# Kernel tuning notes

Measured on AMD Instinct MI355X. Metric: run time of the kernel, lower is better.

Reference implementation:

```python
import jax, jax.numpy as jnp
import numpy as np

B, T, C, H = 4, 4096, 1024, 128

def setup_inputs() -> dict:
    key = jax.random.key(0)
    kx, kq, kk, kv = jax.random.split(key, 4)
    s = 1.0 / np.sqrt(C)  # linear-layer-like init scale
    return {
        "x": jax.random.normal(kx, (B, T, C), dtype=jnp.float32),
        "Wq": jax.random.normal(kq, (C, H), dtype=jnp.float32) * s,
        "Wk": jax.random.normal(kk, (C, H), dtype=jnp.float32) * s,
        "Wv": jax.random.normal(kv, (C, H), dtype=jnp.float32) * s,
    }

def reference(x, Wq, Wk, Wv):
    # q,k,v: [B,T,H]
    q = jnp.einsum('btc,ch->bth', x, Wq)
    k = jnp.einsum('btc,ch->bth', x, Wk)
    v = jnp.einsum('btc,ch->bth', x, Wv)
    # scores: [B,T,T]  (NOTE: source applies no 1/sqrt(H) scaling)
    wei = jnp.einsum('bth,bih->bti', q, k)
    t = x.shape[1]
    causal = jnp.tril(jnp.ones((t, t), dtype=bool))
    wei = jnp.where(causal, wei, -jnp.inf)
    probs = jax.nn.softmax(wei, axis=-1)
    out = jnp.einsum('btj,bjh->bth', probs, v)
    return out
```

## Files before the change

kernel.cpp:

```cpp
#include <hip/hip_runtime.h>

#define B_ 4
#define T_ 4096
#define C_ 1024
#define H_ 128

typedef __attribute__((ext_vector_type(8))) __bf16 bf16x8;
typedef __attribute__((ext_vector_type(8))) unsigned short u16x8;
typedef __attribute__((ext_vector_type(4))) float f32x4;

__device__ __forceinline__ unsigned short f2bf(float f) {
  unsigned int u = __float_as_uint(f);
  return (unsigned short)((u + 0x7FFFu + ((u >> 16) & 1u)) >> 16);
}
__device__ __forceinline__ float bf2f(unsigned short h) {
  return __uint_as_float((unsigned)h << 16);
}
__device__ __forceinline__ bf16x8 ldb8(const unsigned short* p) {
  return *(const bf16x8*)(const void*)p;
}
__device__ __forceinline__ void async16(void* lds, const void* g) {
  __builtin_amdgcn_global_load_lds(
      (const __attribute__((address_space(1))) unsigned int*)g,
      (__attribute__((address_space(3))) unsigned int*)lds, 16, 0, 0);
}
__device__ __forceinline__ void split8a(const float* f, bf16x8& hi, bf16x8& lo) {
  u16x8 h, l;
#pragma unroll
  for (int j = 0; j < 8; j++) {
    h[j] = f2bf(f[j]);
    l[j] = f2bf(f[j] - bf2f(h[j]));
  }
  hi = __builtin_bit_cast(bf16x8, h);
  lo = __builtin_bit_cast(bf16x8, l);
}


__global__ void wt_k(const float* __restrict__ Wq, const float* __restrict__ Wk,
                     const float* __restrict__ Wv, unsigned short* __restrict__ Whi,
                     unsigned short* __restrict__ Wlo) {
  __shared__ float tile[32][33];
  int m = blockIdx.z;
  const float* W = (m == 0) ? Wq : ((m == 1) ? Wk : Wv);
  int c0 = blockIdx.x * 32, h0 = blockIdx.y * 32;
  int tx = threadIdx.x, ty = threadIdx.y;
#pragma unroll
  for (int i = 0; i < 4; i++)
    tile[ty + 8 * i][tx] = W[(size_t)(c0 + ty + 8 * i) * H_ + h0 + tx];
  __syncthreads();
  size_t base = (size_t)m * H_ * C_;
#pragma unroll
  for (int i = 0; i < 4; i++) {
    float f = tile[tx][ty + 8 * i];
    unsigned short hi = f2bf(f);
    int h = h0 + ty + 8 * i;
    int kg = c0 + tx;
    int w0 = kg >> 6, c = (kg >> 3) & 7, e = kg & 7;
    size_t idx = base + (size_t)h * C_ + w0 * 64 + ((c + (h & 7)) & 7) * 8 + e;
    Whi[idx] = hi;
    if (m < 2) Wlo[idx] = f2bf(f - bf2f(hi));
  }
}

__global__ __launch_bounds__(256, 3) void qkv_k(
    const float* __restrict__ x, const unsigned short* __restrict__ Whi,
    const unsigned short* __restrict__ Wlo, unsigned short* __restrict__ Qhi,
    unsigned short* __restrict__ Qlo, unsigned short* __restrict__ Khf,
    unsigned short* __restrict__ Klf, unsigned short* __restrict__ Vf) {
  int m = blockIdx.x % 3;
  int r0 = (blockIdx.x / 3) * 64;
  __shared__ __align__(16) float sx[64 * 64];
  __shared__ __align__(16) unsigned short swh[128 * 64];
  __shared__ __align__(16) unsigned short swl[128 * 64];
  int tid = threadIdx.x;
  int lane = tid & 63, wave = tid >> 6;
  int l15 = lane & 15, quad = lane >> 4;
  const unsigned short* Wmh = Whi + (size_t)m * H_ * C_;
  const unsigned short* Wml = Wlo + (size_t)m * H_ * C_;
  f32x4 acc[8];
#pragma unroll
  for (int n = 0; n < 8; n++) acc[n] = (f32x4){0.f, 0.f, 0.f, 0.f};

  for (int k0 = 0; k0 < C_; k0 += 64) {
    __syncthreads();
#pragma unroll
    for (int i = 0; i < 4; i++) {
      int s = (wave * 4 + i) * 64 + lane;
      {
        int tr = s >> 4, p = s & 15;
        async16((unsigned short*)sx + (size_t)(wave * 4 + i) * 512,
                x + (size_t)(r0 + tr) * C_ + k0 + ((p - tr) & 15) * 4);
      }
      {
        int hr = s >> 3, p = s & 7;
        async16(swh + (size_t)(wave * 4 + i) * 512,
                Wmh + (size_t)hr * C_ + k0 + p * 8);
        if (m < 2)
          async16(swl + (size_t)(wave * 4 + i) * 512,
                  Wml + (size_t)hr * C_ + k0 + p * 8);
      }
    }
    __syncthreads();
#pragma unroll
    for (int kk = 0; kk < 2; kk++) {
      float xa[8];
#pragma unroll
      for (int half = 0; half < 2; half++) {
        int p = (kk * 8 + quad * 2 + half + l15) & 15;
        *(f32x4*)&xa[half * 4] =
            *(const f32x4*)(const void*)(sx + (wave * 16 + l15) * 64 + p * 4);
      }
      bf16x8 ahi, alo;
      split8a(xa, ahi, alo);
      if (m < 2) {
#pragma unroll
        for (int n = 0; n < 8; n++) {
          int p = (kk * 4 + quad + l15) & 7;
          bf16x8 bhi = ldb8(swh + (n * 16 + l15) * 64 + p * 8);
          bf16x8 blo = ldb8(swl + (n * 16 + l15) * 64 + p * 8);
          acc[n] = __builtin_amdgcn_mfma_f32_16x16x32_bf16(ahi, bhi, acc[n], 0, 0, 0);
          acc[n] = __builtin_amdgcn_mfma_f32_16x16x32_bf16(alo, bhi, acc[n], 0, 0, 0);
          acc[n] = __builtin_amdgcn_mfma_f32_16x16x32_bf16(ahi, blo, acc[n], 0, 0, 0);
        }
      } else {
#pragma unroll
        for (int n = 0; n < 8; n++) {
          int p = (kk * 4 + quad + l15) & 7;
          bf16x8 bhi = ldb8(swh + (n * 16 + l15) * 64 + p * 8);
          acc[n] = __builtin_amdgcn_mfma_f32_16x16x32_bf16(ahi, bhi, acc[n], 0, 0, 0);
        }
      }
    }
  }
  int ob = r0 + wave * 16 + quad * 4;
  if (m == 0) {
#pragma unroll
    for (int n8 = 0; n8 < 8; n8++)
#pragma unroll
      for (int r = 0; r < 4; r++) {
        float f = acc[n8][r];
        unsigned short hi = f2bf(f);
        size_t idx = (size_t)(ob + r) * H_ + n8 * 16 + l15;
        Qhi[idx] = hi;
        Qlo[idx] = f2bf(f - bf2f(hi));
      }
  } else if (m == 1) {
#pragma unroll
    for (int n8 = 0; n8 < 8; n8++)
#pragma unroll
      for (int r = 0; r < 4; r++) {
        int gr = ob + r;
        int bb = gr >> 12, t = gr & (T_ - 1);
        int kt = t >> 6, tr = t & 63, nf = tr >> 4, lk = tr & 15;
        int h = n8 * 16 + l15;
        int kkf = h >> 5, qk = (h >> 3) & 3, e = h & 7;
        size_t idx = (size_t)bb * T_ * H_ +
                     (size_t)((kt * 16 + nf * 4 + kkf) * 64 + qk * 16 + lk) * 8 + e;
        float f = acc[n8][r];
        unsigned short hi = f2bf(f);
        Khf[idx] = hi;
        Klf[idx] = f2bf(f - bf2f(hi));
      }
  } else {
#pragma unroll
    for (int n8 = 0; n8 < 8; n8++)
#pragma unroll
      for (int r = 0; r < 4; r++) {
        int gr = ob + r;
        int bb = gr >> 12, t = gr & (T_ - 1);
        int kt = t >> 6, ks = (t >> 5) & 1, qv = (t >> 3) & 3, jj = t & 7;
        size_t idx = (size_t)bb * T_ * H_ +
                     (size_t)((kt * 16 + ks * 8 + n8) * 64 + qv * 16 + l15) * 8 + jj;
        Vf[idx] = f2bf(acc[n8][r]);
      }
  }
}

__device__ __forceinline__ void online_sm(f32x4* s, float* mr, float* lr,
                                          f32x4* o) {
  float mnew[4];
#pragma unroll
  for (int r = 0; r < 4; r++) mnew[r] = fmaxf(s[0][r], s[1][r]);
#pragma unroll
  for (int off = 1; off < 16; off <<= 1)
#pragma unroll
    for (int r = 0; r < 4; r++) mnew[r] = fmaxf(mnew[r], __shfl_xor(mnew[r], off));
  float alpha[4];
#pragma unroll
  for (int r = 0; r < 4; r++) {
    float mi = fmaxf(mr[r], mnew[r]);
    alpha[r] = __expf(mr[r] - mi);
    mr[r] = mi;
  }
#pragma unroll
  for (int n16 = 0; n16 < 2; ++n16)
#pragma unroll
    for (int r = 0; r < 4; r++) s[n16][r] = __expf(s[n16][r] - mr[r]);
  float rs[4];
#pragma unroll
  for (int r = 0; r < 4; r++) rs[r] = s[0][r] + s[1][r];
#pragma unroll
  for (int off = 1; off < 16; off <<= 1)
#pragma unroll
    for (int r = 0; r < 4; r++) rs[r] += __shfl_xor(rs[r], off);
#pragma unroll
  for (int r = 0; r < 4; r++) lr[r] = lr[r] * alpha[r] + rs[r];
#pragma unroll
  for (int n = 0; n < 8; n++)
#pragma unroll
    for (int r = 0; r < 4; r++) o[n][r] *= alpha[r];
}

#define PP2 40
__global__ __launch_bounds__(256, 2) void flash3_k(
    const unsigned short* __restrict__ Qhi, const unsigned short* __restrict__ Qlo,
    const unsigned short* __restrict__ Khf, const unsigned short* __restrict__ Klf,
    const unsigned short* __restrict__ Vf, float* __restrict__ opart,
    float2* __restrict__ mlpart) {
  __shared__ __align__(16) unsigned short skh[2][4096];
  __shared__ __align__(16) unsigned short skl[2][4096];
  __shared__ __align__(16) unsigned short sv[2][4096];
  __shared__ __align__(16) unsigned short pb[4][2][16 * PP2];
  int tid = threadIdx.x;
  int wave = tid >> 6, lane = tid & 63;
  int l15 = lane & 15, quad = lane >> 4;

  int n = blockIdx.x;
  int p = 31 - (n >> 4);
  int g = n & 15;
  int sp = g >> 2, b = g & 3;
  int q0 = p << 7;
  int ktB = sp * (p + 1);
  int nt = p + 1;
  size_t boff = (size_t)b * T_ * H_;
  const unsigned short* Khb = Khf + boff;
  const unsigned short* Klb = Klf + boff;
  const unsigned short* Vb = Vf + boff;

  bf16x8 qh0[4], ql0[4], qh1[4], ql1[4];
  {
    const unsigned short* qrh =
        Qhi + boff + (size_t)(q0 + wave * 32 + l15) * H_ + quad * 8;
    const unsigned short* qrl =
        Qlo + boff + (size_t)(q0 + wave * 32 + l15) * H_ + quad * 8;
#pragma unroll
    for (int kk = 0; kk < 4; kk++) {
      qh0[kk] = ldb8(qrh + kk * 32);
      ql0[kk] = ldb8(qrl + kk * 32);
      qh1[kk] = ldb8(qrh + 16 * H_ + kk * 32);
      ql1[kk] = ldb8(qrl + 16 * H_ + kk * 32);
    }
  }
  f32x4 o0[8], o1[8];
#pragma unroll
  for (int nn = 0; nn < 8; nn++) {
    o0[nn] = (f32x4){0.f, 0.f, 0.f, 0.f};
    o1[nn] = (f32x4){0.f, 0.f, 0.f, 0.f};
  }
  float mr0[4] = {-1e30f, -1e30f, -1e30f, -1e30f};
  float mr1[4] = {-1e30f, -1e30f, -1e30f, -1e30f};
  float lr0[4] = {0.f, 0.f, 0.f, 0.f};
  float lr1[4] = {0.f, 0.f, 0.f, 0.f};

  int rmin = q0 + wave * 32;
  unsigned short* pb0 = pb[wave][0];
  unsigned short* pb1 = pb[wave][1];
  int ch = wave * 2;

#define STAGE(kt32_, d_)                                                        \
  {                                                                             \
    size_t gbase = (size_t)(kt32_)*4096 + (size_t)ch * 512 + (size_t)lane * 8;  \
    async16(&skh[d_][ch * 512], Khb + gbase);                                   \
    async16(&skh[d_][(ch + 1) * 512], Khb + gbase + 512);                       \
    async16(&skl[d_][ch * 512], Klb + gbase);                                   \
    async16(&skl[d_][(ch + 1) * 512], Klb + gbase + 512);                       \
    async16(&sv[d_][ch * 512], Vb + gbase);                                     \
    async16(&sv[d_][(ch + 1) * 512], Vb + gbase + 512);                         \
  }

  STAGE(ktB, 0);
  int cur = 0;
  for (int it = 0; it < nt; ++it) {
    int kt32 = ktB + it;
    if (it + 1 < nt) {
      STAGE(kt32 + 1, cur ^ 1);
      asm volatile("s_waitcnt vmcnt(6)" ::: "memory");
    } else {
      asm volatile("s_waitcnt vmcnt(0)" ::: "memory");
    }
    __builtin_amdgcn_s_barrier();
    int c0k = kt32 << 5;
    bool t1a = (c0k <= rmin + 31);
    bool t0a = (c0k <= rmin + 15);
    if (t1a) {
      f32x4 s0[2], s1[2];
#pragma unroll
      for (int n16 = 0; n16 < 2; ++n16) {
        s0[n16] = (f32x4){0.f, 0.f, 0.f, 0.f};
        s1[n16] = (f32x4){0.f, 0.f, 0.f, 0.f};
      }
#pragma unroll
      for (int n16 = 0; n16 < 2; ++n16) {
        bf16x8 kh[4], kl[4];
#pragma unroll
        for (int kk = 0; kk < 4; kk++) {
          kh[kk] = ldb8(&skh[cur][(n16 * 4 + kk) * 512 + lane * 8]);
          kl[kk] = ldb8(&skl[cur][(n16 * 4 + kk) * 512 + lane * 8]);
        }
#pragma unroll
        for (int kk = 0; kk < 4; kk++) {
          s0[n16] = __builtin_amdgcn_mfma_f32_16x16x32_bf16(qh0[kk], kh[kk], s0[n16], 0, 0, 0);
          s0[n16] = __builtin_amdgcn_mfma_f32_16x16x32_bf16(ql0[kk], kh[kk], s0[n16], 0, 0, 0);
          s0[n16] = __builtin_amdgcn_mfma_f32_16x16x32_bf16(qh0[kk], kl[kk], s0[n16], 0, 0, 0);
          s1[n16] = __builtin_amdgcn_mfma_f32_16x16x32_bf16(qh1[kk], kh[kk], s1[n16], 0, 0, 0);
          s1[n16] = __builtin_amdgcn_mfma_f32_16x16x32_bf16(ql1[kk], kh[kk], s1[n16], 0, 0, 0);
          s1[n16] = __builtin_amdgcn_mfma_f32_16x16x32_bf16(qh1[kk], kl[kk], s1[n16], 0, 0, 0);
        }
      }
      if (c0k + 31 > rmin + 16) {
#pragma unroll
        for (int n16 = 0; n16 < 2; ++n16) {
          int col = c0k + n16 * 16 + l15;
#pragma unroll
          for (int r = 0; r < 4; r++)
            if (col > rmin + 16 + quad * 4 + r) s1[n16][r] = -1e30f;
        }
      }
      if (t0a && c0k + 31 > rmin) {
#pragma unroll
        for (int n16 = 0; n16 < 2; ++n16) {
          int col = c0k + n16 * 16 + l15;
#pragma unroll
          for (int r = 0; r < 4; r++)
            if (col > rmin + quad * 4 + r) s0[n16][r] = -1e30f;
        }
      }
      online_sm(s1, mr1, lr1, o1);
      if (t0a) online_sm(s0, mr0, lr0, o0);
      asm volatile("s_waitcnt lgkmcnt(0)" ::: "memory");
#pragma unroll
      for (int n16 = 0; n16 < 2; ++n16)
#pragma unroll
        for (int r = 0; r < 4; r++)
          pb1[(quad * 4 + r) * PP2 + n16 * 16 + l15] = f2bf(s1[n16][r]);
      if (t0a) {
#pragma unroll
        for (int n16 = 0; n16 < 2; ++n16)
#pragma unroll
          for (int r = 0; r < 4; r++)
            pb0[(quad * 4 + r) * PP2 + n16 * 16 + l15] = f2bf(s0[n16][r]);
      }
      asm volatile("s_waitcnt lgkmcnt(0)" ::: "memory");
      bf16x8 pa1 = ldb8(pb1 + l15 * PP2 + quad * 8);
      bf16x8 pa0;
      if (t0a) pa0 = ldb8(pb0 + l15 * PP2 + quad * 8);
#pragma unroll
      for (int nv = 0; nv < 8; ++nv) {
        bf16x8 vf = ldb8(&sv[cur][nv * 512 + lane * 8]);
        o1[nv] = __builtin_amdgcn_mfma_f32_16x16x32_bf16(pa1, vf, o1[nv], 0, 0, 0);
        if (t0a)
          o0[nv] = __builtin_amdgcn_mfma_f32_16x16x32_bf16(pa0, vf, o0[nv], 0, 0, 0);
      }
    }
    __builtin_amdgcn_s_barrier();
    cur ^= 1;
  }
#undef STAGE

  size_t obase = (size_t)((b * 32 + p) * 4 + sp) * (128 * 128);
  size_t mbase = (size_t)((b * 32 + p) * 4 + sp) * 128;
  int wr0 = wave * 32 + quad * 4;
#pragma unroll
  for (int nn = 0; nn < 8; nn++)
#pragma unroll
    for (int r = 0; r < 4; r++) {
      opart[obase + (size_t)(wr0 + r) * 128 + nn * 16 + l15] = o0[nn][r];
      opart[obase + (size_t)(wr0 + 16 + r) * 128 + nn * 16 + l15] = o1[nn][r];
    }
  if (l15 == 0) {
#pragma unroll
    for (int r = 0; r < 4; r++) {
      mlpart[mbase + wr0 + r] = make_float2(mr0[r], lr0[r]);
      mlpart[mbase + wr0 + 16 + r] = make_float2(mr1[r], lr1[r]);
    }
  }
}

__global__ __launch_bounds__(256) void comb_k(const float* __restrict__ opart,
                                              const float2* __restrict__ mlpart,
                                              float* __restrict__ out) {
  int gid = blockIdx.x * 256 + threadIdx.x;
  int row = gid >> 4;
  int c0 = (gid & 15) << 3;
  int b = row >> 12, t = row & (T_ - 1);
  int p = t >> 7, r = t & 127;
  size_t base = (size_t)(b * 32 + p) * 4;
  float2 ml[4];
#pragma unroll
  for (int s = 0; s < 4; s++) ml[s] = mlpart[base * 128 + s * 128 + r];
  float M = fmaxf(fmaxf(ml[0].x, ml[1].x), fmaxf(ml[2].x, ml[3].x));
  float w[4], L = 0.f;
#pragma unroll
  for (int s = 0; s < 4; s++) {
    w[s] = __expf(ml[s].x - M);
    L += w[s] * ml[s].y;
  }
  float invL = 1.0f / L;
  f32x4 a0 = (f32x4){0.f, 0.f, 0.f, 0.f}, a1 = a0;
#pragma unroll
  for (int s = 0; s < 4; s++) {
    const float* src = opart + (base + s) * (128 * 128) + (size_t)r * 128 + c0;
    a0 += *(const f32x4*)(const void*)src * w[s];
    a1 += *(const f32x4*)(const void*)(src + 4) * w[s];
  }
  float* op = out + ((size_t)b * T_ + t) * H_ + c0;
  *(f32x4*)(void*)op = a0 * invL;
  *(f32x4*)(void*)(op + 4) = a1 * invL;
}

extern "C" void kernel_launch(void* const* d_in, const int* in_sizes, int n_in,
                              void* d_out, int out_size, void* d_ws, size_t ws_size,
                              hipStream_t stream) {
  const float* x  = (const float*)d_in[0];
  const float* Wq = (const float*)d_in[1];
  const float* Wk = (const float*)d_in[2];
  const float* Wv = (const float*)d_in[3];
  const size_t BTH = (size_t)B_ * T_ * H_;
  unsigned short* Whi = (unsigned short*)d_ws;
  unsigned short* Wlo = Whi + 3 * H_ * C_;
  unsigned short* Vf  = Wlo + 2 * H_ * C_;
  unsigned short* Qhi = Vf + BTH;
  unsigned short* Qlo = Qhi + BTH;
  unsigned short* Khf = Qlo + BTH;
  unsigned short* Klf = Khf + BTH;
  float* opart = (float*)(void*)(Klf + BTH);
  float2* mlpart = (float2*)(void*)(opart + 4 * BTH);
  float* out = (float*)d_out;

  wt_k<<<dim3(32, 4, 3), dim3(32, 8), 0, stream>>>(Wq, Wk, Wv, Whi, Wlo);
  qkv_k<<<3 * (B_ * T_ / 64), 256, 0, stream>>>(x, Whi, Wlo, Qhi, Qlo, Khf, Klf, Vf);
  flash3_k<<<512, 256, 0, stream>>>(Qhi, Qlo, Khf, Klf, Vf, opart, mlpart);
  comb_k<<<(B_ * T_ * 16) / 256, 256, 0, stream>>>(opart, mlpart, out);
}
```

Measured before the change: 239.5 us.

## Transpose score MFMA to keep P in registers and drop LDS round-trip

The QK^T MFMA operands are swapped so the score tile comes out transposed. Each lane then owns one query row, so the softmax row max and sum need only two cross-lane shuffles, and P is repacked into the PV A-operand with lane shuffles instead of a write and read through shared memory. It also skips the s0 MFMAs when that half-tile is fully masked, raises wave priority around the MFMA blocks, and reorders the block-to-query-tile mapping to interleave heavy and light tiles. The risks are extra shuffle instructions and the correctness of the new lane mapping.

```diff
diff --git a/kernel.cpp b/kernel.cpp
--- a/kernel.cpp
+++ b/kernel.cpp
@@ -8,6 +8,7 @@
 typedef __attribute__((ext_vector_type(8))) __bf16 bf16x8;
 typedef __attribute__((ext_vector_type(8))) unsigned short u16x8;
 typedef __attribute__((ext_vector_type(4))) float f32x4;
+typedef __attribute__((ext_vector_type(4))) unsigned int u32x4;
 
 __device__ __forceinline__ unsigned short f2bf(float f) {
   unsigned int u = __float_as_uint(f);
@@ -176,43 +177,53 @@
   }
 }
 
-__device__ __forceinline__ void online_sm(f32x4* s, float* mr, float* lr,
-                                          f32x4* o) {
-  float mnew[4];
-#pragma unroll
-  for (int r = 0; r < 4; r++) mnew[r] = fmaxf(s[0][r], s[1][r]);
-#pragma unroll
-  for (int off = 1; off < 16; off <<= 1)
-#pragma unroll
-    for (int r = 0; r < 4; r++) mnew[r] = fmaxf(mnew[r], __shfl_xor(mnew[r], off));
-  float alpha[4];
-#pragma unroll
-  for (int r = 0; r < 4; r++) {
-    float mi = fmaxf(mr[r], mnew[r]);
-    alpha[r] = __expf(mr[r] - mi);
-    mr[r] = mi;
-  }
-#pragma unroll
-  for (int n16 = 0; n16 < 2; ++n16)
-#pragma unroll
-    for (int r = 0; r < 4; r++) s[n16][r] = __expf(s[n16][r] - mr[r]);
-  float rs[4];
-#pragma unroll
-  for (int r = 0; r < 4; r++) rs[r] = s[0][r] + s[1][r];
-#pragma unroll
-  for (int off = 1; off < 16; off <<= 1)
-#pragma unroll
-    for (int r = 0; r < 4; r++) rs[r] += __shfl_xor(rs[r], off);
-#pragma unroll
-  for (int r = 0; r < 4; r++) lr[r] = lr[r] * alpha[r] + rs[r];
-#pragma unroll
-  for (int n = 0; n < 8; n++)
-#pragma unroll
-    for (int r = 0; r < 4; r++) o[n][r] *= alpha[r];
-}
-
-#define PP2 40
-__global__ __launch_bounds__(256, 2) void flash3_k(
+__device__ __forceinline__ bf16x8 sm_tile(f32x4* s, float& mr, float& lr,
+                                          f32x4* o, int lane) {
+  int l15 = lane & 15, quad = lane >> 4;
+  float mx = fmaxf(fmaxf(fmaxf(s[0][0], s[0][1]), fmaxf(s[0][2], s[0][3])),
+                   fmaxf(fmaxf(s[1][0], s[1][1]), fmaxf(s[1][2], s[1][3])));
+  mx = fmaxf(mx, __shfl_xor(mx, 16));
+  mx = fmaxf(mx, __shfl_xor(mx, 32));
+  float mi = fmaxf(mr, mx);
+  float al = __expf(mr - mi);
+  mr = mi;
+#pragma unroll
+  for (int n16 = 0; n16 < 2; n16++)
+#pragma unroll
+    for (int r = 0; r < 4; r++) s[n16][r] = __expf(s[n16][r] - mi);
+  float sum = ((s[0][0] + s[0][1]) + (s[0][2] + s[0][3])) +
+              ((s[1][0] + s[1][1]) + (s[1][2] + s[1][3]));
+  sum += __shfl_xor(sum, 16);
+  sum += __shfl_xor(sum, 32);
+  lr = lr * al + sum;
+  float alo[4];
+#pragma unroll
+  for (int r = 0; r < 4; r++) alo[r] = __shfl(al, quad * 4 + r);
+#pragma unroll
+  for (int nv = 0; nv < 8; nv++)
+#pragma unroll
+    for (int r = 0; r < 4; r++) o[nv][r] *= alo[r];
+  unsigned W[2][2];
+#pragma unroll
+  for (int n16 = 0; n16 < 2; n16++)
+#pragma unroll
+    for (int j = 0; j < 2; j++)
+      W[n16][j] = (unsigned)f2bf(s[n16][2 * j]) |
+                  ((unsigned)f2bf(s[n16][2 * j + 1]) << 16);
+  int base = ((lane >> 4) & 1) * 32 + l15;
+  unsigned A[4];
+#pragma unroll
+  for (int a = 0; a < 4; a++) {
+    int src = base + (a >> 1) * 16;
+    unsigned lo = (unsigned)__shfl((int)W[0][a & 1], src);
+    unsigned hi = (unsigned)__shfl((int)W[1][a & 1], src);
+    A[a] = (lane & 32) ? hi : lo;
+  }
+  u32x4 aw = (u32x4){A[0], A[1], A[2], A[3]};
+  return __builtin_bit_cast(bf16x8, aw);
+}
+
+__global__ __launch_bounds__(256, 2) void flash4_k(
     const unsigned short* __restrict__ Qhi, const unsigned short* __restrict__ Qlo,
     const unsigned short* __restrict__ Khf, const unsigned short* __restrict__ Klf,
     const unsigned short* __restrict__ Vf, float* __restrict__ opart,
@@ -220,13 +231,13 @@
   __shared__ __align__(16) unsigned short skh[2][4096];
   __shared__ __align__(16) unsigned short skl[2][4096];
   __shared__ __align__(16) unsigned short sv[2][4096];
-  __shared__ __align__(16) unsigned short pb[4][2][16 * PP2];
   int tid = threadIdx.x;
   int wave = tid >> 6, lane = tid & 63;
   int l15 = lane & 15, quad = lane >> 4;
 
   int n = blockIdx.x;
-  int p = 31 - (n >> 4);
+  int h = n >> 4;
+  int p = (h < 16) ? (31 - h) : (h - 16);
   int g = n & 15;
   int sp = g >> 2, b = g & 3;
   int q0 = p << 7;
@@ -257,14 +268,9 @@
     o0[nn] = (f32x4){0.f, 0.f, 0.f, 0.f};
     o1[nn] = (f32x4){0.f, 0.f, 0.f, 0.f};
   }
-  float mr0[4] = {-1e30f, -1e30f, -1e30f, -1e30f};
-  float mr1[4] = {-1e30f, -1e30f, -1e30f, -1e30f};
-  float lr0[4] = {0.f, 0.f, 0.f, 0.f};
-  float lr1[4] = {0.f, 0.f, 0.f, 0.f};
+  float mr0 = -1e30f, mr1 = -1e30f, lr0 = 0.f, lr1 = 0.f;
 
   int rmin = q0 + wave * 32;
-  unsigned short* pb0 = pb[wave][0];
-  unsigned short* pb1 = pb[wave][1];
   int ch = wave * 2;
 
 #define STAGE(kt32_, d_)                                                        \
@@ -299,6 +305,7 @@
         s0[n16] = (f32x4){0.f, 0.f, 0.f, 0.f};
         s1[n16] = (f32x4){0.f, 0.f, 0.f, 0.f};
       }
+      __builtin_amdgcn_s_setprio(1);
 #pragma unroll
       for (int n16 = 0; n16 < 2; ++n16) {
         bf16x8 kh[4], kl[4];
@@ -309,51 +316,41 @@
         }
 #pragma unroll
         for (int kk = 0; kk < 4; kk++) {
-          s0[n16] = __builtin_amdgcn_mfma_f32_16x16x32_bf16(qh0[kk], kh[kk], s0[n16], 0, 0, 0);
-          s0[n16] = __builtin_amdgcn_mfma_f32_16x16x32_bf16(ql0[kk], kh[kk], s0[n16], 0, 0, 0);
-          s0[n16] = __builtin_amdgcn_mfma_f32_16x16x32_bf16(qh0[kk], kl[kk], s0[n16], 0, 0, 0);
-          s1[n16] = __builtin_amdgcn_mfma_f32_16x16x32_bf16(qh1[kk], kh[kk], s1[n16], 0, 0, 0);
-          s1[n16] = __builtin_amdgcn_mfma_f32_16x16x32_bf16(ql1[kk], kh[kk], s1[n16], 0, 0, 0);
-          s1[n16] = __builtin_amdgcn_mfma_f32_16x16x32_bf16(qh1[kk], kl[kk], s1[n16], 0, 0, 0);
+          s1[n16] = __builtin_amdgcn_mfma_f32_16x16x32_bf16(kh[kk], qh1[kk], s1[n16], 0, 0, 0);
+          s1[n16] = __builtin_amdgcn_mfma_f32_16x16x32_bf16(kh[kk], ql1[kk], s1[n16], 0, 0, 0);
+          s1[n16] = __builtin_amdgcn_mfma_f32_16x16x32_bf16(kl[kk], qh1[kk], s1[n16], 0, 0, 0);
+          if (t0a) {
+            s0[n16] = __builtin_amdgcn_mfma_f32_16x16x32_bf16(kh[kk], qh0[kk], s0[n16], 0, 0, 0);
+            s0[n16] = __builtin_amdgcn_mfma_f32_16x16x32_bf16(kh[kk], ql0[kk], s0[n16], 0, 0, 0);
+            s0[n16] = __builtin_amdgcn_mfma_f32_16x16x32_bf16(kl[kk], qh0[kk], s0[n16], 0, 0, 0);
+          }
         }
       }
+      __builtin_amdgcn_s_setprio(0);
       if (c0k + 31 > rmin + 16) {
-#pragma unroll
-        for (int n16 = 0; n16 < 2; ++n16) {
-          int col = c0k + n16 * 16 + l15;
-#pragma unroll
-          for (int r = 0; r < 4; r++)
-            if (col > rmin + 16 + quad * 4 + r) s1[n16][r] = -1e30f;
-        }
+        int row1 = rmin + 16 + l15;
+#pragma unroll
+        for (int n16 = 0; n16 < 2; ++n16)
+#pragma unroll
+          for (int r = 0; r < 4; r++) {
+            int col = c0k + n16 * 16 + quad * 4 + r;
+            if (col > row1) s1[n16][r] = -1e30f;
+          }
       }
       if (t0a && c0k + 31 > rmin) {
-#pragma unroll
-        for (int n16 = 0; n16 < 2; ++n16) {
-          int col = c0k + n16 * 16 + l15;
-#pragma unroll
-          for (int r = 0; r < 4; r++)
-            if (col > rmin + quad * 4 + r) s0[n16][r] = -1e30f;
-        }
-      }
-      online_sm(s1, mr1, lr1, o1);
-      if (t0a) online_sm(s0, mr0, lr0, o0);
-      asm volatile("s_waitcnt lgkmcnt(0)" ::: "memory");
-#pragma unroll
-      for (int n16 = 0; n16 < 2; ++n16)
-#pragma unroll
-        for (int r = 0; r < 4; r++)
-          pb1[(quad * 4 + r) * PP2 + n16 * 16 + l15] = f2bf(s1[n16][r]);
-      if (t0a) {
+        int row0 = rmin + l15;
 #pragma unroll
         for (int n16 = 0; n16 < 2; ++n16)
 #pragma unroll
-          for (int r = 0; r < 4; r++)
-            pb0[(quad * 4 + r) * PP2 + n16 * 16 + l15] = f2bf(s0[n16][r]);
-      }
-      asm volatile("s_waitcnt lgkmcnt(0)" ::: "memory");
-      bf16x8 pa1 = ldb8(pb1 + l15 * PP2 + quad * 8);
+          for (int r = 0; r < 4; r++) {
+            int col = c0k + n16 * 16 + quad * 4 + r;
+            if (col > row0) s0[n16][r] = -1e30f;
+          }
+      }
+      bf16x8 pa1 = sm_tile(s1, mr1, lr1, o1, lane);
       bf16x8 pa0;
-      if (t0a) pa0 = ldb8(pb0 + l15 * PP2 + quad * 8);
+      if (t0a) pa0 = sm_tile(s0, mr0, lr0, o0, lane);
+      __builtin_amdgcn_s_setprio(1);
 #pragma unroll
       for (int nv = 0; nv < 8; ++nv) {
         bf16x8 vf = ldb8(&sv[cur][nv * 512 + lane * 8]);
@@ -361,6 +358,7 @@
         if (t0a)
           o0[nv] = __builtin_amdgcn_mfma_f32_16x16x32_bf16(pa0, vf, o0[nv], 0, 0, 0);
       }
+      __builtin_amdgcn_s_setprio(0);
     }
     __builtin_amdgcn_s_barrier();
     cur ^= 1;
@@ -377,12 +375,9 @@
       opart[obase + (size_t)(wr0 + r) * 128 + nn * 16 + l15] = o0[nn][r];
       opart[obase + (size_t)(wr0 + 16 + r) * 128 + nn * 16 + l15] = o1[nn][r];
     }
-  if (l15 == 0) {
-#pragma unroll
-    for (int r = 0; r < 4; r++) {
-      mlpart[mbase + wr0 + r] = make_float2(mr0[r], lr0[r]);
-      mlpart[mbase + wr0 + 16 + r] = make_float2(mr1[r], lr1[r]);
-    }
+  if (quad == 0) {
+    mlpart[mbase + wave * 32 + l15] = make_float2(mr0, lr0);
+    mlpart[mbase + wave * 32 + 16 + l15] = make_float2(mr1, lr1);
   }
 }
 
@@ -439,6 +434,6 @@
 
   wt_k<<<dim3(32, 4, 3), dim3(32, 8), 0, stream>>>(Wq, Wk, Wv, Whi, Wlo);
   qkv_k<<<3 * (B_ * T_ / 64), 256, 0, stream>>>(x, Whi, Wlo, Qhi, Qlo, Khf, Klf, Vf);
-  flash3_k<<<512, 256, 0, stream>>>(Qhi, Qlo, Khf, Klf, Vf, opart, mlpart);
+  flash4_k<<<512, 256, 0, stream>>>(Qhi, Qlo, Khf, Klf, Vf, opart, mlpart);
   comb_k<<<(B_ * T_ * 16) / 256, 256, 0, stream>>>(opart, mlpart, out);
 }
```

Result: faster. 221.8 us (-7.4%).
